# Kernel optimization log

Hardware: AMD Instinct MI355X
Metric: run time of the kernel (lower is better)

## Reference

```python
import jax, jax.numpy as jnp
import numpy as np

B, T, SLATE, D = 256, 16, 20, 256
N_ITEMS, N_USERS = 100000, 10000


def setup_inputs() -> dict:
    key = jax.random.key(0)
    ks = jax.random.split(key, 8)
    s = 1.0 / np.sqrt(D)  # PyTorch GRU/Linear init scale ~ U(-1/sqrt(H), 1/sqrt(H))
    return {
        "item_idxs": jax.random.randint(ks[0], (B, T, SLATE), 0, N_ITEMS),
        "user_idxs": jax.random.randint(ks[1], (B, T), 0, N_USERS),
        "responses": jnp.zeros((B, T, SLATE), jnp.float32),
        "item_table": jax.random.normal(ks[2], (N_ITEMS, D), jnp.float32) * 0.02,
        "user_table": jax.random.normal(ks[3], (N_USERS, D), jnp.float32) * 0.02,
        "W_ih": jax.random.uniform(ks[4], (3 * D, 2 * D), jnp.float32, -s, s),
        "W_hh": jax.random.uniform(ks[5], (3 * D, D), jnp.float32, -s, s),
        "b_ih": jnp.zeros((3 * D,), jnp.float32),
        "b_hh": jnp.zeros((3 * D,), jnp.float32),
        "W_out": jax.random.uniform(ks[6], (1, D), jnp.float32, -s, s),
        "b_out": jnp.zeros((1,), jnp.float32),
    }


def _gru_cell(x, h, W_ih, W_hh, b_ih, b_hh):
    # PyTorch GRUCell math. x: [N, 2D], h: [N, D]
    gi = x @ W_ih.T + b_ih  # [N, 3D]
    gh = h @ W_hh.T + b_hh  # [N, 3D]
    i_r, i_z, i_n = jnp.split(gi, 3, axis=-1)
    h_r, h_z, h_n = jnp.split(gh, 3, axis=-1)
    r = jax.nn.sigmoid(i_r + h_r)
    z = jax.nn.sigmoid(i_z + h_z)
    n = jnp.tanh(i_n + r * h_n)
    return (1.0 - z) * n + z * h


def reference(item_idxs, user_idxs, responses, item_table, user_table,
              W_ih, W_hh, b_ih, b_hh, W_out, b_out):
    # embedding lookup: item_embs [B,T,S,D], user_embs [B,T,D]
    item_embs = item_table[item_idxs]
    user_embs = user_table[user_idxs]
    N = B * T
    e = item_embs.reshape(N, SLATE, D).transpose(1, 0, 2)  # [S, N, D]
    h0 = user_embs.reshape(N, D)
    m0 = jnp.ones((N, 1), item_embs.dtype)  # 'soft' readout multiplier, 1 at step 0

    def step(carry, e_i):
        h, m = carry
        x = jnp.concatenate([e_i, e_i * m], axis=-1)  # [N, 2D]
        h = _gru_cell(x, h, W_ih, W_hh, b_ih, b_hh)
        y = h @ W_out.T + b_out  # [N, 1]
        return (h, jax.nn.sigmoid(y)), y[:, 0]

    _, ys = jax.lax.scan(step, (h0, m0), e)  # ys: [S, N]
    return ys.transpose(1, 0).reshape(B, T, SLATE)
```

## Files before the change

kernel.cpp:

```cpp
#include <hip/hip_runtime.h>
#include <math.h>

#define SLATE 20
#define DD 256
#define NSEQ 4096

typedef __attribute__((ext_vector_type(8))) short bf16x8;
typedef __attribute__((ext_vector_type(4))) float f32x4;
typedef unsigned short u16;
typedef unsigned int u32;

__device__ __forceinline__ u16 f2bf(float f) {
    unsigned u = __float_as_uint(f);
    u += 0x7fff + ((u >> 16) & 1);
    return (u16)(u >> 16);
}
__device__ __forceinline__ float bf2f(u16 h) {
    return __uint_as_float(((unsigned)h) << 16);
}
__device__ __forceinline__ float sigmoidf_(float x) { return 1.f / (1.f + expf(-x)); }

__device__ __forceinline__ void gl_lds16(const void* g, void* l) {
    __builtin_amdgcn_global_load_lds(
        (const __attribute__((address_space(1))) unsigned int*)g,
        (__attribute__((address_space(3))) unsigned int*)l, 16, 0, 0);
}

__global__ void prep_w(const float* __restrict__ W_ih, const float* __restrict__ W_hh,
                       u16* __restrict__ W12, u16* __restrict__ Whh) {
    int i = blockIdx.x * 256 + threadIdx.x;
    if (i < 1536 * 256) {
        int j = i >> 8, k = i & 255;
        float v = (j < 768) ? W_ih[(size_t)j * 512 + k]
                            : W_ih[(size_t)(j - 768) * 512 + 256 + k];
        W12[i] = f2bf(v);
    } else {
        int i2 = i - 1536 * 256;
        Whh[i2] = f2bf(W_hh[i2]);
    }
}

__global__ void gather_e(int s0, const int* __restrict__ idxs, const float* __restrict__ itab,
                         u16* __restrict__ e_bf) {
    int g = blockIdx.x * 256 + threadIdx.x;
    int row = g >> 6, c = g & 63;
    int n = row & (NSEQ - 1), s = s0 + (row >> 12);
    int idx = idxs[n * SLATE + s];
    float4 v = *(const float4*)&itab[(size_t)idx * DD + c * 4];
    ushort4 o;
    o.x = f2bf(v.x); o.y = f2bf(v.y); o.z = f2bf(v.z); o.w = f2bf(v.w);
    *(ushort4*)&e_bf[(size_t)row * DD + c * 4] = o;
}

__global__ __launch_bounds__(256) void gemm_e(
        const u16* __restrict__ e_bf, const u16* __restrict__ W12, u16* __restrict__ Ge) {
    __shared__ u16 A_s[128][32];
    __shared__ u16 B_s[128][32];

    const int tid = threadIdx.x;
    const int w = tid >> 6, l = tid & 63, lm = l & 15, lq = l >> 4;
    const int wm = w & 1, wn = w >> 1;
    const size_t m0 = (size_t)blockIdx.y * 128;
    const size_t n0 = (size_t)blockIdx.x * 128;

    f32x4 acc[4][4];
    f32x4 zero4 = {0.f, 0.f, 0.f, 0.f};
#pragma unroll
    for (int mi = 0; mi < 4; ++mi)
#pragma unroll
        for (int nj = 0; nj < 4; ++nj) acc[mi][nj] = zero4;

    const int srow = w * 16 + (l >> 2);
    const int skc = (l & 3) * 8;
    const u16* gA = e_bf + (m0 + srow) * DD + skc;
    const u16* gB = W12 + (n0 + srow) * DD + skc;
    u16* lA = &A_s[0][0] + w * 512 + l * 8;
    u16* lB = &B_s[0][0] + w * 512 + l * 8;

    for (int kt = 0; kt < 8; ++kt) {
        const int ko = kt * 32;
        gl_lds16(gA + ko, lA);
        gl_lds16(gA + 64 * DD + ko, lA + 2048);
        gl_lds16(gB + ko, lB);
        gl_lds16(gB + 64 * DD + ko, lB + 2048);
        __syncthreads();
        bf16x8 af[4], bfr[4];
#pragma unroll
        for (int mi = 0; mi < 4; ++mi)
            af[mi] = *(const bf16x8*)&A_s[wm * 64 + mi * 16 + lm][lq * 8];
#pragma unroll
        for (int nj = 0; nj < 4; ++nj)
            bfr[nj] = *(const bf16x8*)&B_s[wn * 64 + nj * 16 + lm][lq * 8];
#pragma unroll
        for (int nj = 0; nj < 4; ++nj)
#pragma unroll
            for (int mi = 0; mi < 4; ++mi)
                acc[mi][nj] = __builtin_amdgcn_mfma_f32_16x16x32_bf16(af[mi], bfr[nj], acc[mi][nj], 0, 0, 0);
        __syncthreads();
    }
#pragma unroll
    for (int mi = 0; mi < 4; ++mi)
#pragma unroll
        for (int rr = 0; rr < 4; ++rr) {
            u16* gp = Ge + (m0 + wm * 64 + mi * 16 + lq * 4 + rr) * 1536 + n0 + wn * 64 + lm;
#pragma unroll
            for (int nj = 0; nj < 4; ++nj) gp[nj * 16] = f2bf(acc[mi][nj][rr]);
        }
}

__global__ __launch_bounds__(1024) void seq_kernel(
        int s0, int C,
        const u16* __restrict__ Ge,
        const u16* __restrict__ Whh,
        const int* __restrict__ user_idxs, const float* __restrict__ user_table,
        const float* __restrict__ b_ih, const float* __restrict__ b_hh,
        const float* __restrict__ W_out, const float* __restrict__ b_out,
        float* __restrict__ h_g, float* __restrict__ m_g, float* __restrict__ out)
{
    __shared__ u16   hA[8][16][32];
    __shared__ float gh_s[16][770];
    __shared__ float bias_s[4][256];
    __shared__ float wo_s[256];

    const int tid = threadIdx.x;
    const int w = tid >> 6, l = tid & 63, lm = l & 15, lq = l >> 4;
    const int n0 = blockIdx.x * 16;
    const int nw = n0 + w;

    if (tid < 256) bias_s[0][tid] = b_ih[tid] + b_hh[tid];
    else if (tid < 512)  { int d = tid - 256; bias_s[1][d] = b_ih[256 + d] + b_hh[256 + d]; }
    else if (tid < 768)  { int d = tid - 512; bias_s[2][d] = b_ih[512 + d]; }
    else                 { int d = tid - 768; bias_s[3][d] = b_hh[512 + d]; wo_s[d] = W_out[d]; }

    float h_reg[4];
    float m_w;
    {
        if (s0 == 0) {
            const float* hu = user_table + (size_t)user_idxs[nw] * DD;
            float2 a = *(const float2*)&hu[2 * l];
            float2 b = *(const float2*)&hu[2 * l + 128];
            h_reg[0] = a.x; h_reg[1] = a.y; h_reg[2] = b.x; h_reg[3] = b.y;
            m_w = 1.f;
        } else {
            float2 a = *(const float2*)&h_g[(size_t)nw * DD + 2 * l];
            float2 b = *(const float2*)&h_g[(size_t)nw * DD + 2 * l + 128];
            h_reg[0] = a.x; h_reg[1] = a.y; h_reg[2] = b.x; h_reg[3] = b.y;
            m_w = m_g[nw];
        }
#pragma unroll
        for (int c = 0; c < 2; ++c) {
            int d0 = 2 * l + 128 * c;
            u32 pk = (u32)f2bf(h_reg[2 * c]) | ((u32)f2bf(h_reg[2 * c + 1]) << 16);
            *(u32*)&hA[d0 >> 5][w][d0 & 31] = pk;
        }
    }

    const u16* wbase = Whh + (size_t)(w * 48 + lm) * DD + lq * 8;
    bf16x8 warr[12];
#pragma unroll
    for (int kt = 0; kt < 4; ++kt)
#pragma unroll
        for (int nj = 0; nj < 3; ++nj)
            warr[kt * 3 + nj] = *(const bf16x8*)(wbase + nj * 16 * DD + kt * 32);

    __syncthreads();

    const float bo = b_out[0];

    for (int sc = 0; sc < C; ++sc) {
        u32 ge2[2][6];
        const u32* geb = (const u32*)(Ge + ((size_t)sc * NSEQ + nw) * 1536);
#pragma unroll
        for (int c = 0; c < 2; ++c)
#pragma unroll
            for (int g = 0; g < 6; ++g)
                ge2[c][g] = geb[g * 128 + l + 64 * c];

        f32x4 zero4 = {0.f, 0.f, 0.f, 0.f};
        f32x4 acc[3];
#pragma unroll
        for (int nj = 0; nj < 3; ++nj) acc[nj] = zero4;
#pragma unroll
        for (int kt = 0; kt < 4; ++kt) {
            bf16x8 af = *(const bf16x8*)&hA[kt][lm][lq * 8];
#pragma unroll
            for (int nj = 0; nj < 3; ++nj)
                acc[nj] = __builtin_amdgcn_mfma_f32_16x16x32_bf16(af, warr[kt * 3 + nj], acc[nj], 0, 0, 0);
        }
#pragma unroll
        for (int kt = 4; kt < 8; ++kt) {
            bf16x8 af = *(const bf16x8*)&hA[kt][lm][lq * 8];
#pragma unroll
            for (int nj = 0; nj < 3; ++nj) {
                bf16x8 bfg = *(const bf16x8*)(wbase + nj * 16 * DD + kt * 32);
                acc[nj] = __builtin_amdgcn_mfma_f32_16x16x32_bf16(af, bfg, acc[nj], 0, 0, 0);
            }
        }
#pragma unroll
        for (int nj = 0; nj < 3; ++nj)
#pragma unroll
            for (int rr = 0; rr < 4; ++rr)
                gh_s[lq * 4 + rr][w * 48 + nj * 16 + lm] = acc[nj][rr];
        __syncthreads();

        float yv = 0.f;
#pragma unroll
        for (int c = 0; c < 2; ++c) {
            const int d0 = 2 * l + 128 * c;
            float g1r_lo = bf2f((u16)(ge2[c][0] & 0xffff)), g1r_hi = bf2f((u16)(ge2[c][0] >> 16));
            float g1z_lo = bf2f((u16)(ge2[c][1] & 0xffff)), g1z_hi = bf2f((u16)(ge2[c][1] >> 16));
            float g1n_lo = bf2f((u16)(ge2[c][2] & 0xffff)), g1n_hi = bf2f((u16)(ge2[c][2] >> 16));
            float g2r_lo = bf2f((u16)(ge2[c][3] & 0xffff)), g2r_hi = bf2f((u16)(ge2[c][3] >> 16));
            float g2z_lo = bf2f((u16)(ge2[c][4] & 0xffff)), g2z_hi = bf2f((u16)(ge2[c][4] >> 16));
            float g2n_lo = bf2f((u16)(ge2[c][5] & 0xffff)), g2n_hi = bf2f((u16)(ge2[c][5] >> 16));
            float2 hr2 = *(const float2*)&gh_s[w][d0];
            float2 hz2 = *(const float2*)&gh_s[w][256 + d0];
            float2 hn2 = *(const float2*)&gh_s[w][512 + d0];
            float2 bcr = *(const float2*)&bias_s[0][d0];
            float2 bcz = *(const float2*)&bias_s[1][d0];
            float2 bin = *(const float2*)&bias_s[2][d0];
            float2 bhn = *(const float2*)&bias_s[3][d0];
            float2 wo2 = *(const float2*)&wo_s[d0];

            float r_lo = sigmoidf_(g1r_lo + m_w * g2r_lo + hr2.x + bcr.x);
            float r_hi = sigmoidf_(g1r_hi + m_w * g2r_hi + hr2.y + bcr.y);
            float z_lo = sigmoidf_(g1z_lo + m_w * g2z_lo + hz2.x + bcz.x);
            float z_hi = sigmoidf_(g1z_hi + m_w * g2z_hi + hz2.y + bcz.y);
            float n_lo = tanhf(g1n_lo + m_w * g2n_lo + bin.x + r_lo * (hn2.x + bhn.x));
            float n_hi = tanhf(g1n_hi + m_w * g2n_hi + bin.y + r_hi * (hn2.y + bhn.y));
            float hn_lo = (1.f - z_lo) * n_lo + z_lo * h_reg[2 * c];
            float hn_hi = (1.f - z_hi) * n_hi + z_hi * h_reg[2 * c + 1];
            h_reg[2 * c] = hn_lo; h_reg[2 * c + 1] = hn_hi;
            u32 pk = (u32)f2bf(hn_lo) | ((u32)f2bf(hn_hi) << 16);
            *(u32*)&hA[d0 >> 5][w][d0 & 31] = pk;
            yv += hn_lo * wo2.x + hn_hi * wo2.y;
        }
#pragma unroll
        for (int off = 32; off > 0; off >>= 1) yv += __shfl_xor(yv, off, 64);
        float y = yv + bo;
        if (l == 0) out[(size_t)nw * SLATE + (s0 + sc)] = y;
        m_w = sigmoidf_(y);
        __syncthreads();
    }

#pragma unroll
    for (int c = 0; c < 2; ++c) {
        float2 v; v.x = h_reg[2 * c]; v.y = h_reg[2 * c + 1];
        *(float2*)&h_g[(size_t)nw * DD + 2 * l + 128 * c] = v;
    }
    if (l == 0) m_g[nw] = m_w;
}

extern "C" void kernel_launch(void* const* d_in, const int* in_sizes, int n_in,
                              void* d_out, int out_size, void* d_ws, size_t ws_size,
                              hipStream_t stream) {
    const int*   item_idxs  = (const int*)d_in[0];
    const int*   user_idxs  = (const int*)d_in[1];
    const float* item_table = (const float*)d_in[3];
    const float* user_table = (const float*)d_in[4];
    const float* W_ih       = (const float*)d_in[5];
    const float* W_hh       = (const float*)d_in[6];
    const float* b_ih       = (const float*)d_in[7];
    const float* b_hh       = (const float*)d_in[8];
    const float* W_out      = (const float*)d_in[9];
    const float* b_out      = (const float*)d_in[10];
    float* out = (float*)d_out;

    const size_t fixed = 786432ull + 393216ull + 4194304ull + 16384ull;
    static const int cands[5] = {10, 5, 4, 2, 1};
    int C = 1;
    for (int i = 0; i < 5; ++i) {
        size_t need = (size_t)cands[i] * (12582912ull + 2097152ull) + fixed;
        if (need <= ws_size) { C = cands[i]; break; }
    }

    u16*   Ge   = (u16*)d_ws;
    u16*   e_bf = (u16*)((char*)d_ws + (size_t)C * 12582912ull);
    u16*   W12  = (u16*)((char*)e_bf + (size_t)C * 2097152ull);
    u16*   Whh  = (u16*)((char*)W12 + 786432ull);
    float* h_g  = (float*)((char*)Whh + 393216ull);
    float* m_g  = (float*)((char*)h_g + 4194304ull);

    prep_w<<<2304, 256, 0, stream>>>(W_ih, W_hh, W12, Whh);

    for (int s0 = 0; s0 < SLATE; s0 += C) {
        gather_e<<<C * 1024, 256, 0, stream>>>(s0, item_idxs, item_table, e_bf);
        dim3 gg(12, 32 * C);
        gemm_e<<<gg, 256, 0, stream>>>(e_bf, W12, Ge);
        seq_kernel<<<256, 1024, 0, stream>>>(s0, C, Ge, Whh, user_idxs, user_table,
                                             b_ih, b_hh, W_out, b_out, h_g, m_g, out);
    }
}
```

Before: 451.0 us.

## Fold biases into GEMM epilogue, swizzle hidden LDS, use fast transcendental intrinsics

```diff
diff --git a/kernel.cpp b/kernel.cpp
--- a/kernel.cpp
+++ b/kernel.cpp
@@ -15,10 +15,14 @@
     u += 0x7fff + ((u >> 16) & 1);
     return (u16)(u >> 16);
 }
-__device__ __forceinline__ float bf2f(u16 h) {
-    return __uint_as_float(((unsigned)h) << 16);
-}
-__device__ __forceinline__ float sigmoidf_(float x) { return 1.f / (1.f + expf(-x)); }
+__device__ __forceinline__ float blo(u32 u) { return __uint_as_float(u << 16); }
+__device__ __forceinline__ float bhi(u32 u) { return __uint_as_float(u & 0xffff0000u); }
+__device__ __forceinline__ float sigm_(float x) {
+    return __builtin_amdgcn_rcpf(1.f + __builtin_amdgcn_exp2f(-1.44269504f * x));
+}
+__device__ __forceinline__ float tanh_(float x) {
+    return 1.f - 2.f * __builtin_amdgcn_rcpf(1.f + __builtin_amdgcn_exp2f(2.88539008f * x));
+}
 
 __device__ __forceinline__ void gl_lds16(const void* g, void* l) {
     __builtin_amdgcn_global_load_lds(
@@ -53,7 +57,8 @@
 }
 
 __global__ __launch_bounds__(256) void gemm_e(
-        const u16* __restrict__ e_bf, const u16* __restrict__ W12, u16* __restrict__ Ge) {
+        const u16* __restrict__ e_bf, const u16* __restrict__ W12,
+        const float* __restrict__ b_ih, u16* __restrict__ Ge) {
     __shared__ u16 A_s[128][32];
     __shared__ u16 B_s[128][32];
 
@@ -98,74 +103,77 @@
                 acc[mi][nj] = __builtin_amdgcn_mfma_f32_16x16x32_bf16(af[mi], bfr[nj], acc[mi][nj], 0, 0, 0);
         __syncthreads();
     }
+    float bb[4];
+#pragma unroll
+    for (int nj = 0; nj < 4; ++nj) {
+        int col = (int)n0 + wn * 64 + nj * 16 + lm;
+        bb[nj] = (col < 768) ? b_ih[col] : 0.f;
+    }
 #pragma unroll
     for (int mi = 0; mi < 4; ++mi)
 #pragma unroll
         for (int rr = 0; rr < 4; ++rr) {
             u16* gp = Ge + (m0 + wm * 64 + mi * 16 + lq * 4 + rr) * 1536 + n0 + wn * 64 + lm;
 #pragma unroll
-            for (int nj = 0; nj < 4; ++nj) gp[nj * 16] = f2bf(acc[mi][nj][rr]);
-        }
-}
-
-__global__ __launch_bounds__(1024) void seq_kernel(
+            for (int nj = 0; nj < 4; ++nj) gp[nj * 16] = f2bf(acc[mi][nj][rr] + bb[nj]);
+        }
+}
+
+__device__ __forceinline__ int hA_off(int seq, int kt, int lq2) {
+    int v = ((kt & 3) << 2) | lq2;
+    return kt * 512 + lq2 * 128 + ((seq ^ v) << 3);
+}
+
+__global__ __launch_bounds__(1024, 4) void seq_kernel(
         int s0, int C,
         const u16* __restrict__ Ge,
         const u16* __restrict__ Whh,
         const int* __restrict__ user_idxs, const float* __restrict__ user_table,
-        const float* __restrict__ b_ih, const float* __restrict__ b_hh,
+        const float* __restrict__ b_hh,
         const float* __restrict__ W_out, const float* __restrict__ b_out,
         float* __restrict__ h_g, float* __restrict__ m_g, float* __restrict__ out)
 {
-    __shared__ u16   hA[8][16][32];
+    __shared__ u16   hA[4096];
     __shared__ float gh_s[16][770];
-    __shared__ float bias_s[4][256];
-    __shared__ float wo_s[256];
 
     const int tid = threadIdx.x;
     const int w = tid >> 6, l = tid & 63, lm = l & 15, lq = l >> 4;
     const int n0 = blockIdx.x * 16;
     const int nw = n0 + w;
-
-    if (tid < 256) bias_s[0][tid] = b_ih[tid] + b_hh[tid];
-    else if (tid < 512)  { int d = tid - 256; bias_s[1][d] = b_ih[256 + d] + b_hh[256 + d]; }
-    else if (tid < 768)  { int d = tid - 512; bias_s[2][d] = b_ih[512 + d]; }
-    else                 { int d = tid - 768; bias_s[3][d] = b_hh[512 + d]; wo_s[d] = W_out[d]; }
-
-    float h_reg[4];
-    float m_w;
-    {
-        if (s0 == 0) {
-            const float* hu = user_table + (size_t)user_idxs[nw] * DD;
-            float2 a = *(const float2*)&hu[2 * l];
-            float2 b = *(const float2*)&hu[2 * l + 128];
-            h_reg[0] = a.x; h_reg[1] = a.y; h_reg[2] = b.x; h_reg[3] = b.y;
-            m_w = 1.f;
-        } else {
-            float2 a = *(const float2*)&h_g[(size_t)nw * DD + 2 * l];
-            float2 b = *(const float2*)&h_g[(size_t)nw * DD + 2 * l + 128];
-            h_reg[0] = a.x; h_reg[1] = a.y; h_reg[2] = b.x; h_reg[3] = b.y;
-            m_w = m_g[nw];
-        }
-#pragma unroll
-        for (int c = 0; c < 2; ++c) {
-            int d0 = 2 * l + 128 * c;
-            u32 pk = (u32)f2bf(h_reg[2 * c]) | ((u32)f2bf(h_reg[2 * c + 1]) << 16);
-            *(u32*)&hA[d0 >> 5][w][d0 & 31] = pk;
-        }
-    }
-
-    const u16* wbase = Whh + (size_t)(w * 48 + lm) * DD + lq * 8;
-    bf16x8 warr[12];
-#pragma unroll
-    for (int kt = 0; kt < 4; ++kt)
-#pragma unroll
-        for (int nj = 0; nj < 3; ++nj)
-            warr[kt * 3 + nj] = *(const bf16x8*)(wbase + nj * 16 * DD + kt * 32);
-
+    const int jw = w * 48;
+
+    const u16* wbase = Whh + (size_t)(jw + lm) * DD + lq * 8;
+    bf16x8 warr0[8], warr1[8];
+#pragma unroll
+    for (int kt = 0; kt < 8; ++kt) {
+        warr0[kt] = *(const bf16x8*)(wbase + kt * 32);
+        warr1[kt] = *(const bf16x8*)(wbase + 16 * DD + kt * 32);
+    }
+    const u16* wb2 = wbase + 32 * DD;
+
+    float bhh0 = b_hh[jw + lm], bhh1 = b_hh[jw + 16 + lm], bhh2 = b_hh[jw + 32 + lm];
+    float2 woA = *(const float2*)&W_out[2 * l];
+    float2 woB = *(const float2*)&W_out[2 * l + 128];
+    const float bo = b_out[0];
+
+    float h_reg[4]; float m_w;
+    if (s0 == 0) {
+        const float* hu = user_table + (size_t)user_idxs[nw] * DD;
+        float2 a = *(const float2*)&hu[2 * l];
+        float2 b = *(const float2*)&hu[2 * l + 128];
+        h_reg[0] = a.x; h_reg[1] = a.y; h_reg[2] = b.x; h_reg[3] = b.y; m_w = 1.f;
+    } else {
+        float2 a = *(const float2*)&h_g[(size_t)nw * DD + 2 * l];
+        float2 b = *(const float2*)&h_g[(size_t)nw * DD + 2 * l + 128];
+        h_reg[0] = a.x; h_reg[1] = a.y; h_reg[2] = b.x; h_reg[3] = b.y; m_w = m_g[nw];
+    }
+#pragma unroll
+    for (int c = 0; c < 2; ++c) {
+        int kt = (l >> 4) + 4 * c, lq2 = (l >> 2) & 3;
+        u32 pk = (u32)f2bf(h_reg[2 * c]) | ((u32)f2bf(h_reg[2 * c + 1]) << 16);
+        *(u32*)&hA[hA_off(w, kt, lq2) + 2 * (l & 3)] = pk;
+    }
     __syncthreads();
-
-    const float bo = b_out[0];
 
     for (int sc = 0; sc < C; ++sc) {
         u32 ge2[2][6];
@@ -177,69 +185,56 @@
                 ge2[c][g] = geb[g * 128 + l + 64 * c];
 
         f32x4 zero4 = {0.f, 0.f, 0.f, 0.f};
-        f32x4 acc[3];
-#pragma unroll
-        for (int nj = 0; nj < 3; ++nj) acc[nj] = zero4;
-#pragma unroll
-        for (int kt = 0; kt < 4; ++kt) {
-            bf16x8 af = *(const bf16x8*)&hA[kt][lm][lq * 8];
-#pragma unroll
-            for (int nj = 0; nj < 3; ++nj)
-                acc[nj] = __builtin_amdgcn_mfma_f32_16x16x32_bf16(af, warr[kt * 3 + nj], acc[nj], 0, 0, 0);
-        }
-#pragma unroll
-        for (int kt = 4; kt < 8; ++kt) {
-            bf16x8 af = *(const bf16x8*)&hA[kt][lm][lq * 8];
-#pragma unroll
-            for (int nj = 0; nj < 3; ++nj) {
-                bf16x8 bfg = *(const bf16x8*)(wbase + nj * 16 * DD + kt * 32);
-                acc[nj] = __builtin_amdgcn_mfma_f32_16x16x32_bf16(af, bfg, acc[nj], 0, 0, 0);
-            }
-        }
-#pragma unroll
-        for (int nj = 0; nj < 3; ++nj)
-#pragma unroll
-            for (int rr = 0; rr < 4; ++rr)
-                gh_s[lq * 4 + rr][w * 48 + nj * 16 + lm] = acc[nj][rr];
+        f32x4 acc0 = zero4, acc1 = zero4, acc2 = zero4;
+#pragma unroll
+        for (int kt = 0; kt < 8; ++kt) {
+            bf16x8 af = *(const bf16x8*)&hA[hA_off(lm, kt, lq)];
+            acc0 = __builtin_amdgcn_mfma_f32_16x16x32_bf16(af, warr0[kt], acc0, 0, 0, 0);
+            acc1 = __builtin_amdgcn_mfma_f32_16x16x32_bf16(af, warr1[kt], acc1, 0, 0, 0);
+            bf16x8 b2 = *(const bf16x8*)(wb2 + kt * 32);
+            acc2 = __builtin_amdgcn_mfma_f32_16x16x32_bf16(af, b2, acc2, 0, 0, 0);
+        }
+#pragma unroll
+        for (int rr = 0; rr < 4; ++rr) {
+            gh_s[lq * 4 + rr][jw + lm]      = acc0[rr] + bhh0;
+            gh_s[lq * 4 + rr][jw + 16 + lm] = acc1[rr] + bhh1;
+            gh_s[lq * 4 + rr][jw + 32 + lm] = acc2[rr] + bhh2;
+        }
         __syncthreads();
 
         float yv = 0.f;
 #pragma unroll
         for (int c = 0; c < 2; ++c) {
             const int d0 = 2 * l + 128 * c;
-            float g1r_lo = bf2f((u16)(ge2[c][0] & 0xffff)), g1r_hi = bf2f((u16)(ge2[c][0] >> 16));
-            float g1z_lo = bf2f((u16)(ge2[c][1] & 0xffff)), g1z_hi = bf2f((u16)(ge2[c][1] >> 16));
-            float g1n_lo = bf2f((u16)(ge2[c][2] & 0xffff)), g1n_hi = bf2f((u16)(ge2[c][2] >> 16));
-            float g2r_lo = bf2f((u16)(ge2[c][3] & 0xffff)), g2r_hi = bf2f((u16)(ge2[c][3] >> 16));
-            float g2z_lo = bf2f((u16)(ge2[c][4] & 0xffff)), g2z_hi = bf2f((u16)(ge2[c][4] >> 16));
-            float g2n_lo = bf2f((u16)(ge2[c][5] & 0xffff)), g2n_hi = bf2f((u16)(ge2[c][5] >> 16));
-            float2 hr2 = *(const float2*)&gh_s[w][d0];
-            float2 hz2 = *(const float2*)&gh_s[w][256 + d0];
-            float2 hn2 = *(const float2*)&gh_s[w][512 + d0];
-            float2 bcr = *(const float2*)&bias_s[0][d0];
-            float2 bcz = *(const float2*)&bias_s[1][d0];
-            float2 bin = *(const float2*)&bias_s[2][d0];
-            float2 bhn = *(const float2*)&bias_s[3][d0];
-            float2 wo2 = *(const float2*)&wo_s[d0];
-
-            float r_lo = sigmoidf_(g1r_lo + m_w * g2r_lo + hr2.x + bcr.x);
-            float r_hi = sigmoidf_(g1r_hi + m_w * g2r_hi + hr2.y + bcr.y);
-            float z_lo = sigmoidf_(g1z_lo + m_w * g2z_lo + hz2.x + bcz.x);
-            float z_hi = sigmoidf_(g1z_hi + m_w * g2z_hi + hz2.y + bcz.y);
-            float n_lo = tanhf(g1n_lo + m_w * g2n_lo + bin.x + r_lo * (hn2.x + bhn.x));
-            float n_hi = tanhf(g1n_hi + m_w * g2n_hi + bin.y + r_hi * (hn2.y + bhn.y));
-            float hn_lo = (1.f - z_lo) * n_lo + z_lo * h_reg[2 * c];
-            float hn_hi = (1.f - z_hi) * n_hi + z_hi * h_reg[2 * c + 1];
+            float2 ghr = *(const float2*)&gh_s[w][d0];
+            float2 ghz = *(const float2*)&gh_s[w][256 + d0];
+            float2 ghn = *(const float2*)&gh_s[w][512 + d0];
+            float ir_lo = fmaf(m_w, blo(ge2[c][3]), blo(ge2[c][0]));
+            float ir_hi = fmaf(m_w, bhi(ge2[c][3]), bhi(ge2[c][0]));
+            float iz_lo = fmaf(m_w, blo(ge2[c][4]), blo(ge2[c][1]));
+            float iz_hi = fmaf(m_w, bhi(ge2[c][4]), bhi(ge2[c][1]));
+            float in_lo = fmaf(m_w, blo(ge2[c][5]), blo(ge2[c][2]));
+            float in_hi = fmaf(m_w, bhi(ge2[c][5]), bhi(ge2[c][2]));
+            float r_lo = sigm_(ir_lo + ghr.x);
+            float r_hi = sigm_(ir_hi + ghr.y);
+            float z_lo = sigm_(iz_lo + ghz.x);
+            float z_hi = sigm_(iz_hi + ghz.y);
+            float n_lo = tanh_(fmaf(r_lo, ghn.x, in_lo));
+            float n_hi = tanh_(fmaf(r_hi, ghn.y, in_hi));
+            float hn_lo = fmaf(z_lo, h_reg[2 * c] - n_lo, n_lo);
+            float hn_hi = fmaf(z_hi, h_reg[2 * c + 1] - n_hi, n_hi);
             h_reg[2 * c] = hn_lo; h_reg[2 * c + 1] = hn_hi;
+            int kt = (l >> 4) + 4 * c, lq2 = (l >> 2) & 3;
             u32 pk = (u32)f2bf(hn_lo) | ((u32)f2bf(hn_hi) << 16);
-            *(u32*)&hA[d0 >> 5][w][d0 & 31] = pk;
+            *(u32*)&hA[hA_off(w, kt, lq2) + 2 * (l & 3)] = pk;
+            float2 wo2 = c ? woB : woA;
             yv += hn_lo * wo2.x + hn_hi * wo2.y;
         }
 #pragma unroll
         for (int off = 32; off > 0; off >>= 1) yv += __shfl_xor(yv, off, 64);
         float y = yv + bo;
         if (l == 0) out[(size_t)nw * SLATE + (s0 + sc)] = y;
-        m_w = sigmoidf_(y);
+        m_w = sigm_(y);
         __syncthreads();
     }
 
@@ -286,8 +281,8 @@
     for (int s0 = 0; s0 < SLATE; s0 += C) {
         gather_e<<<C * 1024, 256, 0, stream>>>(s0, item_idxs, item_table, e_bf);
         dim3 gg(12, 32 * C);
-        gemm_e<<<gg, 256, 0, stream>>>(e_bf, W12, Ge);
+        gemm_e<<<gg, 256, 0, stream>>>(e_bf, W12, b_ih, Ge);
         seq_kernel<<<256, 1024, 0, stream>>>(s0, C, Ge, Whh, user_idxs, user_table,
-                                             b_ih, b_hh, W_out, b_out, h_g, m_g, out);
-    }
-}
+                                             b_hh, W_out, b_out, h_g, m_g, out);
+    }
+}
```

Result: no change. 443.7 us (-1.6%).
